# Kernel optimization log

Hardware: AMD Instinct MI355X
Metric: run time of the kernel (lower is better)

## Reference

```python
import jax, jax.numpy as jnp
import numpy as np

D = 4096
B = 2
S = 2048


def setup_inputs() -> dict:
    key = jax.random.key(0)
    k1, k2, k3, k4 = jax.random.split(key, 4)
    x = jax.random.normal(k1, (B, S, D), dtype=jnp.float32)
    # 2-bit symmetric quantized codes stored as uint8 in torch; torch's
    # clamp(-1,1).to(uint8) wraps -1 -> 255, so codes span {0,1,255}-like
    # values. We draw the full uint8 range for a representative baseline.
    q_int = jax.random.randint(k2, (D, D), 0, 256, dtype=jnp.int32)
    # per-channel positive scales (small, like 2-bit scales: |w|max / 1)
    scale = jax.random.uniform(k3, (D,), dtype=jnp.float32) * 0.01 + 1e-4
    # symmetric quantization -> zero_point = 0 per channel (int buffer)
    zero_point = jnp.zeros((D,), dtype=jnp.int32)
    bias = jax.random.normal(k4, (D,), dtype=jnp.float32) * 0.02
    return {"x": x, "q_int": q_int, "scale": scale,
            "zero_point": zero_point, "bias": bias}


def reference(x, q_int, scale, zero_point, bias):
    # Faithful to FFQLinear.forward:
    #   weight = (q_int.float() - zero_point) * scale
    # NOTE: no unsqueeze(-1) here (unlike pack time), so scale/zp broadcast
    # over the LAST (column) axis of the [d, d] code matrix.
    zp = zero_point.astype(jnp.float32)
    W = (q_int.astype(jnp.float32) - zp[None, :]) * scale[None, :]  # [D, D]
    b, s, d = x.shape
    # F.linear(x2d, W.t(), bias) == x2d @ W + bias
    out = jnp.einsum('bsd,dk->bsk', x, W) + bias  # [B, S, D]
    return out
```

## Files before the change

### kernel.cpp

```cpp
#include <hip/hip_runtime.h>
#include <stdint.h>

typedef unsigned short u16;
typedef __attribute__((ext_vector_type(8))) short short8;
typedef __attribute__((ext_vector_type(4))) float f32x4;

#define KD 4096

typedef const __attribute__((address_space(1))) void* gas1_t;
typedef __attribute__((address_space(3))) void* las3_t;

__device__ __forceinline__ void g2l16(const void* g, void* l) {
  __builtin_amdgcn_global_load_lds((gas1_t)g, (las3_t)l, 16, 0, 0);
}

__device__ __forceinline__ u16 f2bf(float f) {
  uint32_t u = __float_as_uint(f);
  return (u16)((u + 0x7FFFu + ((u >> 16) & 1u)) >> 16);
}

__global__ __launch_bounds__(256)
void cvt_fused(const float4* __restrict__ x, const int* __restrict__ q,
               const int* __restrict__ zp, uint2* __restrict__ xb,
               u16* __restrict__ qt) {
  const int b = blockIdx.x;
  if (b >= 4096) {
    int gid = (b - 4096) * 256 + threadIdx.x;
    float4 f = x[gid];
    union { u16 u[4]; uint2 v; } o;
    o.u[0] = f2bf(f.x); o.u[1] = f2bf(f.y);
    o.u[2] = f2bf(f.z); o.u[3] = f2bf(f.w);
    xb[gid] = o.v;
    return;
  }
  __shared__ uint32_t P[32][68];
  const int n0 = (b & 63) * 64;
  const int k0 = (b >> 6) * 64;
  const int nc = threadIdx.x & 15;
  const int kr = threadIdx.x >> 4;

  int z[4];
#pragma unroll
  for (int j = 0; j < 4; ++j) z[j] = zp[n0 + nc * 4 + j];

#pragma unroll
  for (int s = 0; s < 2; ++s) {
    const int kp = kr + s * 16;
    const int64_t rb = (int64_t)(k0 + kp * 2) * KD + n0 + nc * 4;
    int4 r0 = *(const int4*)(q + rb);
    int4 r1 = *(const int4*)(q + rb + KD);
    uint4 w;
    w.x = (uint32_t)f2bf((float)(r0.x - z[0])) | ((uint32_t)f2bf((float)(r1.x - z[0])) << 16);
    w.y = (uint32_t)f2bf((float)(r0.y - z[1])) | ((uint32_t)f2bf((float)(r1.y - z[1])) << 16);
    w.z = (uint32_t)f2bf((float)(r0.z - z[2])) | ((uint32_t)f2bf((float)(r1.z - z[2])) << 16);
    w.w = (uint32_t)f2bf((float)(r0.w - z[3])) | ((uint32_t)f2bf((float)(r1.w - z[3])) << 16);
    *(uint4*)&P[kp][nc * 4] = w;
  }
  __syncthreads();

  const int kq = threadIdx.x & 7;
  const int nn = threadIdx.x >> 3;
#pragma unroll
  for (int p = 0; p < 2; ++p) {
    const int n = nn + p * 32;
    uint4 v;
    v.x = P[kq * 4 + 0][n];
    v.y = P[kq * 4 + 1][n];
    v.z = P[kq * 4 + 2][n];
    v.w = P[kq * 4 + 3][n];
    *(uint4*)(qt + (int64_t)(n0 + n) * KD + k0 + kq * 8) = v;
  }
}

__global__ __launch_bounds__(512, 2)
void gemm8(const u16* __restrict__ A, const u16* __restrict__ Bt,
           const float* __restrict__ scale, const float* __restrict__ bias,
           float* __restrict__ C) {
  __shared__ u16 lds[65536];

  const int tid = threadIdx.x;
  const int orig = blockIdx.x;
  const int lid = (orig & 7) * 32 + (orig >> 3);
  const int bm0 = (lid >> 4) * 256;
  const int bn0 = (lid & 15) * 256;

  const int lane = tid & 63;
  const int w = tid >> 6;
  const int wr = w >> 2;
  const int wc = w & 3;
  const int l15 = lane & 15;
  const int q4 = lane >> 4;
  const int l7 = l15 & 7;

  const int rl = tid >> 3;
  const int csw = (tid & 7) ^ (rl & 7);
  const u16* gA = A + (int64_t)(bm0 + rl) * KD + csw * 8;
  const u16* gB = Bt + (int64_t)(bn0 + rl) * KD + csw * 8;

#define STA(b_, qq, kt) g2l16(gA + (int64_t)(qq) * 64 * KD + (kt), &lds[(b_) * 32768 + (qq) * 4096 + tid * 8])
#define STB(b_, qq, kt) g2l16(gB + (int64_t)(qq) * 64 * KD + (kt), &lds[16384 + (b_) * 32768 + (qq) * 4096 + tid * 8])

#define RD_A(mh)                                                              \
  do {                                                                        \
    _Pragma("unroll") for (int m = 0; m < 4; ++m) {                           \
      const int row = wr * 128 + (mh) * 64 + m * 16 + l15;                    \
      _Pragma("unroll") for (int kk = 0; kk < 2; ++kk)                        \
        ar[m][kk] = *(const short8*)&Ab[row * 64 + (((kk * 4 + q4) ^ l7) * 8)]; \
    }                                                                         \
  } while (0)

#define RD_B(nn0)                                                             \
  do {                                                                        \
    _Pragma("unroll") for (int n = 0; n < 2; ++n) {                           \
      const int col = wc * 64 + ((nn0) + n) * 16 + l15;                       \
      _Pragma("unroll") for (int kk = 0; kk < 2; ++kk)                        \
        br[(nn0) + n][kk] = *(const short8*)&Bb[col * 64 + (((kk * 4 + q4) ^ l7) * 8)]; \
    }                                                                         \
  } while (0)

#define MFMA_Q(mb, nn0)                                                       \
  do {                                                                        \
    __builtin_amdgcn_s_setprio(1);                                            \
    _Pragma("unroll") for (int m = 0; m < 4; ++m)                             \
      _Pragma("unroll") for (int n = 0; n < 2; ++n)                           \
        _Pragma("unroll") for (int kk = 0; kk < 2; ++kk)                      \
          acc[(mb) + m][(nn0) + n] = __builtin_amdgcn_mfma_f32_16x16x32_bf16( \
              ar[m][kk], br[(nn0) + n][kk], acc[(mb) + m][(nn0) + n], 0, 0, 0); \
    __builtin_amdgcn_s_setprio(0);                                            \
  } while (0)

#define BAR __builtin_amdgcn_s_barrier()
#define SCHED0 __builtin_amdgcn_sched_barrier(0)
#define CFENCE asm volatile("" ::: "memory")
#define VMC8 asm volatile("s_waitcnt vmcnt(8)" ::: "memory")
#define VMC0 asm volatile("s_waitcnt vmcnt(0)" ::: "memory")

  f32x4 acc[8][4];
#pragma unroll
  for (int m = 0; m < 8; ++m)
#pragma unroll
    for (int n = 0; n < 4; ++n) acc[m][n] = (f32x4)(0.f);

  short8 ar[4][2], br[4][2];

  STB(0, 0, 0); STB(0, 1, 0); STB(0, 2, 0); STB(0, 3, 0);
  STA(0, 0, 0); STA(0, 1, 0); STA(0, 2, 0); STA(0, 3, 0);

  int cur = 0;
  for (int t = 0; t < 63; ++t) {
    const int ktn = (t + 1) * 64;
    const u16* __restrict__ Ab = &lds[cur * 32768];
    const u16* __restrict__ Bb = &lds[16384 + cur * 32768];
    const int nb = cur ^ 1;

    SCHED0; CFENCE;
    BAR;
    STB(nb, 0, ktn); STB(nb, 1, ktn); STB(nb, 2, ktn); STB(nb, 3, ktn);
    STA(nb, 0, ktn); STA(nb, 1, ktn); STA(nb, 2, ktn); STA(nb, 3, ktn);
    VMC8;
    BAR;
    SCHED0; CFENCE;

    RD_A(0);
    RD_B(0);
    RD_B(2);
    MFMA_Q(0, 0);
    MFMA_Q(0, 2);
    RD_A(1);
    MFMA_Q(4, 0);
    MFMA_Q(4, 2);

    cur ^= 1;
  }

  {
    const u16* __restrict__ Ab = &lds[cur * 32768];
    const u16* __restrict__ Bb = &lds[16384 + cur * 32768];
    SCHED0; CFENCE;
    BAR;
    VMC0;
    BAR;
    SCHED0; CFENCE;
    RD_A(0);
    RD_B(0);
    RD_B(2);
    MFMA_Q(0, 0);
    MFMA_Q(0, 2);
    RD_A(1);
    MFMA_Q(4, 0);
    MFMA_Q(4, 2);
  }

  const int r4 = q4 * 4;
#pragma unroll
  for (int n = 0; n < 4; ++n) {
    const int col = bn0 + wc * 64 + n * 16 + l15;
    const float sc = scale[col];
    const float bs = bias[col];
#pragma unroll
    for (int mi = 0; mi < 8; ++mi) {
      const int row = bm0 + wr * 128 + mi * 16 + r4;
#pragma unroll
      for (int j = 0; j < 4; ++j)
        C[(int64_t)(row + j) * KD + col] = acc[mi][n][j] * sc + bs;
    }
  }
}

extern "C" void kernel_launch(void* const* d_in, const int* in_sizes, int n_in,
                              void* d_out, int out_size, void* d_ws, size_t ws_size,
                              hipStream_t stream) {
  const float* x = (const float*)d_in[0];
  const int* q = (const int*)d_in[1];
  const float* scale = (const float*)d_in[2];
  const int* zp = (const int*)d_in[3];
  const float* bias = (const float*)d_in[4];
  float* out = (float*)d_out;

  u16* Xb = (u16*)d_ws;
  u16* Qt = Xb + (size_t)4096 * 4096;

  cvt_fused<<<20480, 256, 0, stream>>>((const float4*)x, q, zp,
                                       (uint2*)Xb, Qt);

  gemm8<<<256, 512, 0, stream>>>(Xb, Qt, scale, bias, out);
}
```

Baseline: 288.0 us.

## Interleave global-to-LDS prefetch with MFMA phases using fine-grained waitcnt barriers

Replaces the double-buffered K loop, which issued all eight prefetch loads up front and then waited, with a four-phase K tile. Each phase issues part of the next tile's global_load_lds, reads LDS fragments, waits on lgkmcnt and vmcnt at partial counts, and runs one MFMA quarter between barriers. The loop is unrolled by two with constant LDS offsets, removing buffer-index arithmetic. This aims to spread memory traffic across compute phases and keep MFMAs fed, at the cost of many more workgroup barriers per tile and fragile hand-tuned wait counts.

```diff
diff --git a/kernel.cpp b/kernel.cpp
--- a/kernel.cpp
+++ b/kernel.cpp
@@ -97,24 +97,24 @@
   const u16* gA = A + (int64_t)(bm0 + rl) * KD + csw * 8;
   const u16* gB = Bt + (int64_t)(bn0 + rl) * KD + csw * 8;
 
-#define STA(b_, qq, kt) g2l16(gA + (int64_t)(qq) * 64 * KD + (kt), &lds[(b_) * 32768 + (qq) * 4096 + tid * 8])
-#define STB(b_, qq, kt) g2l16(gB + (int64_t)(qq) * 64 * KD + (kt), &lds[16384 + (b_) * 32768 + (qq) * 4096 + tid * 8])
-
-#define RD_A(mh)                                                              \
+#define STA(OFF, qq, kt) g2l16(gA + (int64_t)(qq) * 64 * KD + (kt), &lds[(OFF) + (qq) * 4096 + tid * 8])
+#define STB(OFF, qq, kt) g2l16(gB + (int64_t)(qq) * 64 * KD + (kt), &lds[(OFF) + (qq) * 4096 + tid * 8])
+
+#define RD_A(AOFF, mh)                                                        \
   do {                                                                        \
     _Pragma("unroll") for (int m = 0; m < 4; ++m) {                           \
       const int row = wr * 128 + (mh) * 64 + m * 16 + l15;                    \
       _Pragma("unroll") for (int kk = 0; kk < 2; ++kk)                        \
-        ar[m][kk] = *(const short8*)&Ab[row * 64 + (((kk * 4 + q4) ^ l7) * 8)]; \
+        ar[m][kk] = *(const short8*)&lds[(AOFF) + row * 64 + (((kk * 4 + q4) ^ l7) * 8)]; \
     }                                                                         \
   } while (0)
 
-#define RD_B(nn0)                                                             \
+#define RD_B(BOFF, nn0)                                                       \
   do {                                                                        \
     _Pragma("unroll") for (int n = 0; n < 2; ++n) {                           \
       const int col = wc * 64 + ((nn0) + n) * 16 + l15;                       \
       _Pragma("unroll") for (int kk = 0; kk < 2; ++kk)                        \
-        br[(nn0) + n][kk] = *(const short8*)&Bb[col * 64 + (((kk * 4 + q4) ^ l7) * 8)]; \
+        br[(nn0) + n][kk] = *(const short8*)&lds[(BOFF) + col * 64 + (((kk * 4 + q4) ^ l7) * 8)]; \
     }                                                                         \
   } while (0)
 
@@ -131,9 +131,42 @@
 
 #define BAR __builtin_amdgcn_s_barrier()
 #define SCHED0 __builtin_amdgcn_sched_barrier(0)
-#define CFENCE asm volatile("" ::: "memory")
-#define VMC8 asm volatile("s_waitcnt vmcnt(8)" ::: "memory")
+#define LGKM0 do { asm volatile("s_waitcnt lgkmcnt(0)" ::: "memory"); SCHED0; } while (0)
+#define LGKM8 asm volatile("s_waitcnt lgkmcnt(8)" ::: "memory")
+#define VMC6 asm volatile("s_waitcnt vmcnt(6)" ::: "memory")
+#define VMC2 asm volatile("s_waitcnt vmcnt(2)" ::: "memory")
 #define VMC0 asm volatile("s_waitcnt vmcnt(0)" ::: "memory")
+#define WNONE
+
+#define K_TILE(AOFF, BOFF, SAOFF, SBOFF, KTN, STG, W1, W2)                    \
+  do {                                                                        \
+                                                                     \
+    RD_A(AOFF, 0);                                                            \
+    RD_B(BOFF, 0);                                                            \
+    if (STG) { STB(SBOFF, 0, KTN); STB(SBOFF, 1, KTN); STA(SAOFF, 0, KTN); }  \
+    LGKM8;                                                                    \
+    BAR; LGKM0;                                                               \
+    MFMA_Q(0, 0);                                                             \
+    BAR;                                                                      \
+                                                                     \
+    RD_B(BOFF, 2);                                                            \
+    if (STG) { STB(SBOFF, 2, KTN); STB(SBOFF, 3, KTN); STA(SAOFF, 2, KTN); }  \
+    W1;                                                                       \
+    BAR; LGKM0;                                                               \
+    MFMA_Q(0, 2);                                                             \
+    BAR;                                                                      \
+                                                                     \
+    RD_A(AOFF, 1);                                                            \
+    if (STG) { STA(SAOFF, 1, KTN); STA(SAOFF, 3, KTN); }                      \
+    BAR; LGKM0;                                                               \
+    MFMA_Q(4, 0);                                                             \
+    BAR;                                                                      \
+                                                                     \
+    W2;                                                                       \
+    BAR; LGKM0;                                                               \
+    MFMA_Q(4, 2);                                                             \
+    BAR;                                                                      \
+  } while (0)
 
   f32x4 acc[8][4];
 #pragma unroll
@@ -143,53 +176,20 @@
 
   short8 ar[4][2], br[4][2];
 
-  STB(0, 0, 0); STB(0, 1, 0); STB(0, 2, 0); STB(0, 3, 0);
-  STA(0, 0, 0); STA(0, 1, 0); STA(0, 2, 0); STA(0, 3, 0);
-
-  int cur = 0;
-  for (int t = 0; t < 63; ++t) {
-    const int ktn = (t + 1) * 64;
-    const u16* __restrict__ Ab = &lds[cur * 32768];
-    const u16* __restrict__ Bb = &lds[16384 + cur * 32768];
-    const int nb = cur ^ 1;
-
-    SCHED0; CFENCE;
-    BAR;
-    STB(nb, 0, ktn); STB(nb, 1, ktn); STB(nb, 2, ktn); STB(nb, 3, ktn);
-    STA(nb, 0, ktn); STA(nb, 1, ktn); STA(nb, 2, ktn); STA(nb, 3, ktn);
-    VMC8;
-    BAR;
-    SCHED0; CFENCE;
-
-    RD_A(0);
-    RD_B(0);
-    RD_B(2);
-    MFMA_Q(0, 0);
-    MFMA_Q(0, 2);
-    RD_A(1);
-    MFMA_Q(4, 0);
-    MFMA_Q(4, 2);
-
-    cur ^= 1;
-  }
-
-  {
-    const u16* __restrict__ Ab = &lds[cur * 32768];
-    const u16* __restrict__ Bb = &lds[16384 + cur * 32768];
-    SCHED0; CFENCE;
-    BAR;
-    VMC0;
-    BAR;
-    SCHED0; CFENCE;
-    RD_A(0);
-    RD_B(0);
-    RD_B(2);
-    MFMA_Q(0, 0);
-    MFMA_Q(0, 2);
-    RD_A(1);
-    MFMA_Q(4, 0);
-    MFMA_Q(4, 2);
-  }
+  STB(16384, 0, 0); STB(16384, 1, 0); STA(0, 0, 0);
+  STB(16384, 2, 0); STB(16384, 3, 0); STA(0, 2, 0);
+  STA(0, 1, 0); STA(0, 3, 0);
+  VMC2;
+  BAR;
+
+  for (int i = 0; i < 31; ++i) {
+    const int kt1 = (2 * i + 1) * 64;
+    const int kt2 = (2 * i + 2) * 64;
+    K_TILE(0, 16384, 32768, 49152, kt1, 1, VMC6, VMC2);
+    K_TILE(32768, 49152, 0, 16384, kt2, 1, VMC6, VMC2);
+  }
+  K_TILE(0, 16384, 32768, 49152, 63 * 64, 1, VMC6, VMC2);
+  K_TILE(32768, 49152, 0, 16384, 0, 0, VMC0, WNONE);
 
   const int r4 = q4 * 4;
 #pragma unroll
```

New measurement: 279.2 us. 1.03x faster.
